# Kernel optimization log

Hardware: AMD Instinct MI355X
Metric: run time of the kernel (lower is better)

## Reference

```python
import jax, jax.numpy as jnp
import numpy as np

TEMPERATURE = 0.1
WINDOW = 7  # torch loop: k in range(1, min(8, seq_len - i)) -> offsets 1..7


def _normalize(x, axis=-1, eps=1e-12):
    # F.normalize: x / max(||x||, eps)
    n = jnp.linalg.norm(x, axis=axis, keepdims=True)
    return x / jnp.maximum(n, eps)


def setup_inputs() -> dict:
    key = jax.random.key(0)
    k1, k2 = jax.random.split(key, 2)
    states = jax.random.normal(k1, (4, 16, 1024, 256), dtype=jnp.float32)
    patterns = jax.random.normal(k2, (64, 256), dtype=jnp.float32)
    transfer_weights = jnp.zeros((16, 64, 64), dtype=jnp.float32)
    return {"states": states, "patterns": patterns, "transfer_weights": transfer_weights}


def _forward(states, patterns, transfer_weights):
    b, h, s, d = states.shape
    # --- detect_patterns: similarity to normalized pattern library + softmax ---
    sims = jnp.einsum('bhsd,pd->bhsp', states, _normalize(patterns))
    pattern_scores = jax.nn.softmax(sims / TEMPERATURE, axis=-1)  # [b,h,s,p]

    # --- compute_routing_scores: grad of states.sum() wrt states is ones ->
    #     grad_norm = ||ones||_2 over dim = sqrt(d) (constant), softmax over seq ---
    grad_norm = jnp.full((b, h, s), jnp.sqrt(jnp.float32(d)), dtype=states.dtype)
    routing_scores = jax.nn.softmax(grad_norm / TEMPERATURE, axis=-1)  # uniform [b,h,s]

    # --- optimize_routing: windowed min-plus shortest-path DP ---
    # torch keeps distances [b,h,s,s] but every slice along dim 2 is identical
    # (init and updates only index the last axis), so carry a [b,h,s] vector
    # and broadcast at the end. Pad by WINDOW so near-end updates land in pad.
    inf = jnp.float32(np.inf)
    dist0 = jnp.full((b, h, s + WINDOW), inf, dtype=states.dtype).at[..., 0].set(0.0)
    cost_pad = jnp.pad(-routing_scores, ((0, 0), (0, 0), (0, WINDOW)))

    def step(dist, i):
        cur = jax.lax.dynamic_slice_in_dim(dist, i, 1, axis=-1)          # [b,h,1]
        win = jax.lax.dynamic_slice_in_dim(dist, i + 1, WINDOW, axis=-1)  # [b,h,W]
        c = jax.lax.dynamic_slice_in_dim(cost_pad, i + 1, WINDOW, axis=-1)
        new = jnp.minimum(win, cur + c)
        dist = jax.lax.dynamic_update_slice_in_dim(dist, new, i + 1, axis=-1)
        return dist, None

    dist, _ = jax.lax.scan(step, dist0, jnp.arange(s - 1))
    d_final = dist[..., :s]                                  # [b,h,s]
    optimal_routes = jnp.broadcast_to(d_final[:, :, None, :], (b, h, s, s))

    return routing_scores, optimal_routes, transfer_weights, pattern_scores


def reference(states, patterns, transfer_weights):
    return _forward(states, patterns, transfer_weights)
```

## Files before the change

kernel.cpp:

```cpp
#include <hip/hip_runtime.h>
#include <math.h>

constexpr int B = 4, H = 16, S = 1024, D = 256, P = 64;
constexpr long long N_ROWS = (long long)B * H * S;
constexpr long long OFF_RT = 0;
constexpr long long SZ_RT  = N_ROWS;
constexpr long long OFF_OR = OFF_RT + SZ_RT;
constexpr long long SZ_OR  = N_ROWS * (long long)S;
constexpr long long OFF_TW = OFF_OR + SZ_OR;
constexpr long long SZ_TW  = 16LL * 64 * 64;
constexpr long long OFF_PS = OFF_TW + SZ_TW;

typedef _Float16 half8   __attribute__((ext_vector_type(8)));
typedef _Float16 half4v  __attribute__((ext_vector_type(4)));
typedef float    floatx4 __attribute__((ext_vector_type(4)));

constexpr int BSTRIDE = 264;

__global__ __launch_bounds__(256) void k_fill_prep(
        floatx4* __restrict__ routes,
        const floatx4* __restrict__ tw,
        float* __restrict__ out,
        const float* __restrict__ pat,
        _Float16* __restrict__ pnh,
        _Float16* __restrict__ pnl) {
    long long blk = blockIdx.x;
    int t = threadIdx.x;
    if (blk < 65536) {
        long long i = blk * 256 + t;
        int j0 = (int)((i << 2) & (S - 1));
        float b0 = (float)j0 * (-0.0009765625f);
        floatx4 v;
        v.x = b0;
        v.y = b0 - 0.0009765625f;
        v.z = b0 - 0.001953125f;
        v.w = b0 - 0.0029296875f;
        routes[i] = v;
    } else if (blk < 65536 + 128) {
        int i = (int)(blk - 65536) * 256 + t;
        constexpr int Q = (int)SZ_RT / 4;
        if (i < Q) {
            floatx4 v = { 0.0009765625f, 0.0009765625f,
                          0.0009765625f, 0.0009765625f };
            ((floatx4*)(out + OFF_RT))[i] = v;
        } else {
            ((floatx4*)(out + OFF_TW))[i - Q] = tw[i - Q];
        }
    } else {
        int p    = (int)(blk - 65536 - 128) * 4 + (t >> 6);
        int lane = t & 63;
        const floatx4* src = (const floatx4*)(pat + (long long)p * D);
        floatx4 v = src[lane];
        float ss = v.x * v.x + v.y * v.y + v.z * v.z + v.w * v.w;
        #pragma unroll
        for (int m = 1; m < 64; m <<= 1) ss += __shfl_xor(ss, m, 64);
        float scale = 10.0f / fmaxf(sqrtf(ss), 1e-12f);
        float a[4] = { v.x * scale, v.y * scale, v.z * scale, v.w * scale };
        half4v hh, ll;
        #pragma unroll
        for (int j = 0; j < 4; ++j) {
            _Float16 h = (_Float16)a[j];
            hh[j] = h;
            ll[j] = (_Float16)(a[j] - (float)h);
        }
        *(half4v*)(pnh + (long long)p * D + lane * 4) = hh;
        *(half4v*)(pnl + (long long)p * D + lane * 4) = ll;
    }
}

__global__ __launch_bounds__(256) void k_gemm_mfma(
        const float* __restrict__ states,
        const _Float16* __restrict__ pnh,
        const _Float16* __restrict__ pnl,
        float* __restrict__ out_ps) {
    __shared__ _Float16 smem[2 * P * BSTRIDE];
    _Float16* smH = smem;
    _Float16* smL = smem + P * BSTRIDE;

    int tid  = threadIdx.x;
    {
        const half8* gh = (const half8*)pnh;
        const half8* gl = (const half8*)pnl;
        #pragma unroll
        for (int it = 0; it < 8; ++it) {
            int idx = it * 256 + tid;
            int row = idx >> 5;
            int c8  = idx & 31;
            *(half8*)&smH[row * BSTRIDE + c8 * 8] = gh[idx];
            *(half8*)&smL[row * BSTRIDE + c8 * 8] = gl[idx];
        }
    }
    __syncthreads();

    int wave = tid >> 6;
    int lane = tid & 63;
    int q    = lane >> 4;
    int m    = lane & 15;
    long long row0 = (long long)blockIdx.x * 128 + wave * 32;
    const float* __restrict__ arow0 = states + (row0 + m) * D + q * 8;
    const float* __restrict__ arow1 = arow0 + 16 * D;

    floatx4 acc0[4] = {floatx4{0,0,0,0}, floatx4{0,0,0,0},
                       floatx4{0,0,0,0}, floatx4{0,0,0,0}};
    floatx4 acc1[4] = {floatx4{0,0,0,0}, floatx4{0,0,0,0},
                       floatx4{0,0,0,0}, floatx4{0,0,0,0}};

    float4 n0 = *(const float4*)(arow0);
    float4 n1 = *(const float4*)(arow0 + 4);
    float4 n2 = *(const float4*)(arow1);
    float4 n3 = *(const float4*)(arow1 + 4);
    #pragma unroll
    for (int kk = 0; kk < 8; ++kk) {
        float av0[8] = { n0.x, n0.y, n0.z, n0.w, n1.x, n1.y, n1.z, n1.w };
        float av1[8] = { n2.x, n2.y, n2.z, n2.w, n3.x, n3.y, n3.z, n3.w };
        if (kk < 7) {
            n0 = *(const float4*)(arow0 + (kk + 1) * 32);
            n1 = *(const float4*)(arow0 + (kk + 1) * 32 + 4);
            n2 = *(const float4*)(arow1 + (kk + 1) * 32);
            n3 = *(const float4*)(arow1 + (kk + 1) * 32 + 4);
        }
        half8 ah0, al0, ah1, al1;
        #pragma unroll
        for (int j = 0; j < 8; ++j) {
            _Float16 h0 = (_Float16)av0[j];
            ah0[j] = h0;
            al0[j] = (_Float16)(av0[j] - (float)h0);
            _Float16 h1 = (_Float16)av1[j];
            ah1[j] = h1;
            al1[j] = (_Float16)(av1[j] - (float)h1);
        }
        #pragma unroll
        for (int t = 0; t < 4; ++t) {
            int boff = (t * 16 + m) * BSTRIDE + kk * 32 + q * 8;
            half8 bh = *(const half8*)&smH[boff];
            half8 bl = *(const half8*)&smL[boff];
            acc0[t] = __builtin_amdgcn_mfma_f32_16x16x32_f16(ah0, bh, acc0[t], 0, 0, 0);
            acc0[t] = __builtin_amdgcn_mfma_f32_16x16x32_f16(al0, bh, acc0[t], 0, 0, 0);
            acc0[t] = __builtin_amdgcn_mfma_f32_16x16x32_f16(ah0, bl, acc0[t], 0, 0, 0);
            acc1[t] = __builtin_amdgcn_mfma_f32_16x16x32_f16(ah1, bh, acc1[t], 0, 0, 0);
            acc1[t] = __builtin_amdgcn_mfma_f32_16x16x32_f16(al1, bh, acc1[t], 0, 0, 0);
            acc1[t] = __builtin_amdgcn_mfma_f32_16x16x32_f16(ah1, bl, acc1[t], 0, 0, 0);
        }
    }

    #pragma unroll
    for (int set = 0; set < 2; ++set) {
        floatx4* acc = set ? acc1 : acc0;
        long long rbase = row0 + set * 16;
        #pragma unroll
        for (int r = 0; r < 4; ++r) {
            float mx = fmaxf(fmaxf(acc[0][r], acc[1][r]),
                             fmaxf(acc[2][r], acc[3][r]));
            #pragma unroll
            for (int msk = 1; msk < 16; msk <<= 1)
                mx = fmaxf(mx, __shfl_xor(mx, msk, 64));
            float e[4];
            float s = 0.0f;
            #pragma unroll
            for (int t = 0; t < 4; ++t) { e[t] = __expf(acc[t][r] - mx); s += e[t]; }
            #pragma unroll
            for (int msk = 1; msk < 16; msk <<= 1) s += __shfl_xor(s, msk, 64);
            float inv = 1.0f / s;
            long long row = rbase + q * 4 + r;
            #pragma unroll
            for (int t = 0; t < 4; ++t) {
                out_ps[row * P + t * 16 + m] = e[t] * inv;
            }
        }
    }
}

extern "C" void kernel_launch(void* const* d_in, const int* in_sizes, int n_in,
                              void* d_out, int out_size, void* d_ws, size_t ws_size,
                              hipStream_t stream) {
    const float* states   = (const float*)d_in[0];
    const float* patterns = (const float*)d_in[1];
    const float* transfer = (const float*)d_in[2];
    float* out = (float*)d_out;
    _Float16* pnh = (_Float16*)d_ws;
    _Float16* pnl = pnh + P * D;

    k_fill_prep<<<dim3(65536 + 128 + 16), dim3(256), 0, stream>>>(
        (floatx4*)(out + OFF_OR), (const floatx4*)transfer, out,
        patterns, pnh, pnl);

    k_gemm_mfma<<<dim3(512), dim3(256), 0, stream>>>(states, pnh, pnl, out + OFF_PS);
}
```

Measured before the change: 322.8 us.

## Fuse route fill, pattern normalization and MFMA GEMM into one heterogeneous launch

Merges the two kernels into a single launch. GEMM blocks now normalize the patterns into LDS themselves instead of reading a workspace, so the workspace round-trip and the inter-kernel dependency go away. Filler blocks for the huge routes output each write sixteen float4s per thread, which cuts the block count from 65536 to 4096. The GEMM and the fills can now overlap, at the cost of every GEMM block redundantly recomputing the 64 pattern norms and a larger LDS footprint for the filler blocks.

```diff
diff --git a/kernel.cpp b/kernel.cpp
--- a/kernel.cpp
+++ b/kernel.cpp
@@ -17,86 +17,80 @@
 
 constexpr int BSTRIDE = 264;
 
-__global__ __launch_bounds__(256) void k_fill_prep(
-        floatx4* __restrict__ routes,
+constexpr int GEMM_BLOCKS  = 512;
+constexpr int SMALL_BLOCKS = 128;
+constexpr int ROUTE_F4_PER_THREAD = 16;
+constexpr int ROUTE_BLOCKS =
+    (int)((SZ_OR / 4) / (256LL * ROUTE_F4_PER_THREAD));
+
+__global__ __launch_bounds__(256) void k_fused(
+        const float* __restrict__ states,
+        const float* __restrict__ pat,
         const floatx4* __restrict__ tw,
-        float* __restrict__ out,
-        const float* __restrict__ pat,
-        _Float16* __restrict__ pnh,
-        _Float16* __restrict__ pnl) {
-    long long blk = blockIdx.x;
-    int t = threadIdx.x;
-    if (blk < 65536) {
-        long long i = blk * 256 + t;
-        int j0 = (int)((i << 2) & (S - 1));
-        float b0 = (float)j0 * (-0.0009765625f);
-        floatx4 v;
-        v.x = b0;
-        v.y = b0 - 0.0009765625f;
-        v.z = b0 - 0.001953125f;
-        v.w = b0 - 0.0029296875f;
-        routes[i] = v;
-    } else if (blk < 65536 + 128) {
-        int i = (int)(blk - 65536) * 256 + t;
-        constexpr int Q = (int)SZ_RT / 4;
-        if (i < Q) {
-            floatx4 v = { 0.0009765625f, 0.0009765625f,
-                          0.0009765625f, 0.0009765625f };
-            ((floatx4*)(out + OFF_RT))[i] = v;
+        float* __restrict__ out) {
+    __shared__ _Float16 smem[2 * P * BSTRIDE];
+    int blk = blockIdx.x;
+    int tid = threadIdx.x;
+
+    if (blk >= GEMM_BLOCKS) {
+        if (blk < GEMM_BLOCKS + SMALL_BLOCKS) {
+            int i = (blk - GEMM_BLOCKS) * 256 + tid;
+            constexpr int Q = (int)(SZ_RT / 4);
+            if (i < Q) {
+                floatx4 v = { 0.0009765625f, 0.0009765625f,
+                              0.0009765625f, 0.0009765625f };
+                ((floatx4*)(out + OFF_RT))[i] = v;
+            } else {
+                ((floatx4*)(out + OFF_TW))[i - Q] = tw[i - Q];
+            }
         } else {
-            ((floatx4*)(out + OFF_TW))[i - Q] = tw[i - Q];
+            long long rb = blk - GEMM_BLOCKS - SMALL_BLOCKS;
+            float b0 = (float)(tid << 2) * (-0.0009765625f);
+            floatx4 v;
+            v.x = b0;
+            v.y = b0 - 0.0009765625f;
+            v.z = b0 - 0.001953125f;
+            v.w = b0 - 0.0029296875f;
+            floatx4* dst = (floatx4*)(out + OFF_OR)
+                         + rb * (256LL * ROUTE_F4_PER_THREAD) + tid;
+            #pragma unroll
+            for (int k = 0; k < ROUTE_F4_PER_THREAD; ++k)
+                dst[k * 256] = v;
         }
-    } else {
-        int p    = (int)(blk - 65536 - 128) * 4 + (t >> 6);
-        int lane = t & 63;
-        const floatx4* src = (const floatx4*)(pat + (long long)p * D);
-        floatx4 v = src[lane];
+        return;
+    }
+
+    _Float16* smH = smem;
+    _Float16* smL = smem + P * BSTRIDE;
+
+    int tid_ = tid;
+    int wave = tid_ >> 6;
+    int lane = tid_ & 63;
+
+    #pragma unroll 4
+    for (int i = 0; i < 16; ++i) {
+        int p = wave * 16 + i;
+        floatx4 v = ((const floatx4*)(pat + (long long)p * D))[lane];
         float ss = v.x * v.x + v.y * v.y + v.z * v.z + v.w * v.w;
         #pragma unroll
         for (int m = 1; m < 64; m <<= 1) ss += __shfl_xor(ss, m, 64);
         float scale = 10.0f / fmaxf(sqrtf(ss), 1e-12f);
-        float a[4] = { v.x * scale, v.y * scale, v.z * scale, v.w * scale };
         half4v hh, ll;
         #pragma unroll
         for (int j = 0; j < 4; ++j) {
-            _Float16 h = (_Float16)a[j];
+            float a = v[j] * scale;
+            _Float16 h = (_Float16)a;
             hh[j] = h;
-            ll[j] = (_Float16)(a[j] - (float)h);
+            ll[j] = (_Float16)(a - (float)h);
         }
-        *(half4v*)(pnh + (long long)p * D + lane * 4) = hh;
-        *(half4v*)(pnl + (long long)p * D + lane * 4) = ll;
-    }
-}
-
-__global__ __launch_bounds__(256) void k_gemm_mfma(
-        const float* __restrict__ states,
-        const _Float16* __restrict__ pnh,
-        const _Float16* __restrict__ pnl,
-        float* __restrict__ out_ps) {
-    __shared__ _Float16 smem[2 * P * BSTRIDE];
-    _Float16* smH = smem;
-    _Float16* smL = smem + P * BSTRIDE;
-
-    int tid  = threadIdx.x;
-    {
-        const half8* gh = (const half8*)pnh;
-        const half8* gl = (const half8*)pnl;
-        #pragma unroll
-        for (int it = 0; it < 8; ++it) {
-            int idx = it * 256 + tid;
-            int row = idx >> 5;
-            int c8  = idx & 31;
-            *(half8*)&smH[row * BSTRIDE + c8 * 8] = gh[idx];
-            *(half8*)&smL[row * BSTRIDE + c8 * 8] = gl[idx];
-        }
+        *(half4v*)&smH[p * BSTRIDE + lane * 4] = hh;
+        *(half4v*)&smL[p * BSTRIDE + lane * 4] = ll;
     }
     __syncthreads();
 
-    int wave = tid >> 6;
-    int lane = tid & 63;
-    int q    = lane >> 4;
-    int m    = lane & 15;
-    long long row0 = (long long)blockIdx.x * 128 + wave * 32;
+    int q = lane >> 4;
+    int m = lane & 15;
+    long long row0 = (long long)blk * 128 + wave * 32;
     const float* __restrict__ arow0 = states + (row0 + m) * D + q * 8;
     const float* __restrict__ arow1 = arow0 + 16 * D;
 
@@ -143,6 +137,7 @@
         }
     }
 
+    float* out_ps = out + OFF_PS;
     #pragma unroll
     for (int set = 0; set < 2; ++set) {
         floatx4* acc = set ? acc1 : acc0;
@@ -177,12 +172,7 @@
     const float* patterns = (const float*)d_in[1];
     const float* transfer = (const float*)d_in[2];
     float* out = (float*)d_out;
-    _Float16* pnh = (_Float16*)d_ws;
-    _Float16* pnl = pnh + P * D;
 
-    k_fill_prep<<<dim3(65536 + 128 + 16), dim3(256), 0, stream>>>(
-        (floatx4*)(out + OFF_OR), (const floatx4*)transfer, out,
-        patterns, pnh, pnl);
-
-    k_gemm_mfma<<<dim3(512), dim3(256), 0, stream>>>(states, pnh, pnl, out + OFF_PS);
+    k_fused<<<dim3(GEMM_BLOCKS + SMALL_BLOCKS + ROUTE_BLOCKS), dim3(256), 0,
+              stream>>>(states, patterns, (const floatx4*)transfer, out);
 }
```

Result: slower. 343.4 us (+6.4%).
